# Kernel optimization log

Measured on AMD Instinct MI355X. Metric: run time of the kernel, lower is better.

Reference implementation:

```python
import jax, jax.numpy as jnp
import numpy as np
import math

B, N, D, O, H = 2, 3072, 64, 64, 4

def setup_inputs() -> dict:
    key = jax.random.key(0)
    ks = jax.random.split(key, 8)
    x = jax.random.normal(ks[0], (B, N, D), dtype=jnp.float32)
    edge_index = jax.random.randint(ks[1], (B, N, N), 0, 2, dtype=jnp.int32)
    s = 1.0 / math.sqrt(D)
    Wv = jax.random.uniform(ks[2], (H, D, O), jnp.float32, -s, s)
    bv = jax.random.uniform(ks[3], (H, O), jnp.float32, -s, s)
    Wq = jax.random.uniform(ks[4], (H, D, O), jnp.float32, -s, s)
    bq = jax.random.uniform(ks[5], (H, O), jnp.float32, -s, s)
    Wk = jax.random.uniform(ks[6], (H, D, O), jnp.float32, -s, s)
    bk = jax.random.uniform(ks[7], (H, O), jnp.float32, -s, s)
    return {"x": x, "edge_index": edge_index, "Wv": Wv, "bv": bv,
            "Wq": Wq, "bq": bq, "Wk": Wk, "bk": bk}

def reference(x, edge_index, Wv, bv, Wq, bq, Wk, bk):
    # x: [B,N,D]; edge_index: dense {0,1} adjacency [B,N,N]
    dk = jnp.asarray(math.sqrt(x.shape[-1]), x.dtype)
    v = jnp.einsum('bnd,hdo->bhno', x, Wv) + bv[None, :, None, :]
    q = jnp.einsum('bnd,hdo->bhno', x, Wq) + bq[None, :, None, :]
    k = jnp.einsum('bnd,hdo->bhno', x, Wk) + bk[None, :, None, :]
    scores = jnp.einsum('bhno,bhmo->bhnm', q, k) / dk        # [B,H,N,N]
    scores = jax.nn.leaky_relu(scores, 0.2)
    mask = (-1e10) * (1.0 - edge_index.astype(scores.dtype))  # [B,N,N]
    scores = scores + mask[:, None, :, :]
    prop = jax.nn.softmax(scores, axis=-1)
    # dropout on v omitted (inference mode: identity)
    feats = jnp.einsum('bhnm,bhmo->bhno', prop, v)            # [B,H,N,O]
    out = jnp.mean(feats, axis=1)                             # [B,N,O]
    return jax.nn.leaky_relu(out, 0.2)
```

## Files before the change

### kernel.cpp

```cpp
#include <hip/hip_runtime.h>
#include <hip/hip_bf16.h>
#include <cstdint>

#define Bc 2
#define Nc 3072
#define Hc 4
#define NW32 96
#define TILEB 8192
#define KSC 8
#define TPS (NW32/KSC)

typedef __bf16    bf16x8 __attribute__((ext_vector_type(8)));
typedef _Float16  f16x8  __attribute__((ext_vector_type(8)));
typedef float     f32x16 __attribute__((ext_vector_type(16)));

#define QSCALE 0.18033688f

static __device__ __forceinline__ f32x16 mfma32bf(bf16x8 a, bf16x8 b, f32x16 c) {
    return __builtin_amdgcn_mfma_f32_32x32x16_bf16(a, b, c, 0, 0, 0);
}
static __device__ __forceinline__ f32x16 mfma32h(f16x8 a, f16x8 b, f32x16 c) {
    return __builtin_amdgcn_mfma_f32_32x32x16_f16(a, b, c, 0, 0, 0);
}
static __device__ __forceinline__ uint32_t pkrtz(float lo, float hi) {
    uint32_t w;
    asm("v_cvt_pkrtz_f16_f32 %0, %1, %2" : "=v"(w) : "v"(lo), "v"(hi));
    return w;
}

static __device__ __forceinline__ void softmax_pack(const f32x16& sc, uint32_t mwh,
                                                    uint32_t W8[8], float& lsum,
                                                    uint32_t ones32)
{
    #pragma unroll
    for (int i = 0; i < 8; ++i) {
        const int bp0 = (2*i & 3) + 8*(2*i >> 2);
        float s0 = sc[2*i], s1 = sc[2*i + 1];
        float a0 = fmaxf(s0, 0.2f*s0);
        float a1 = fmaxf(s1, 0.2f*s1);
        float e0, e1;
        asm("v_exp_f32 %0, %1" : "=v"(e0) : "v"(a0));
        asm("v_exp_f32 %0, %1" : "=v"(e1) : "v"(a1));
        uint32_t pk = pkrtz(e0, e1);
        uint32_t m0 = (uint32_t)(((int)(mwh << (31 - bp0))) >> 31);
        uint32_t m1 = (uint32_t)(((int)(mwh << (30 - bp0))) >> 31);
        uint32_t wv = pk & ((m0 & 0x0000ffffu) | (m1 & 0xffff0000u));
        W8[i] = wv;
        asm("v_dot2_f32_f16 %0, %1, %2, %0" : "+v"(lsum) : "v"(wv), "v"(ones32));
    }
}

static __device__ __forceinline__ void assemble_pa(uint32_t W8[8], f16x8& pa0, f16x8& pa1)
{
    uint32_t a0 = W8[0], a2 = W8[2], a1 = W8[1], a3 = W8[3];
    uint32_t b0 = W8[4], b2 = W8[6], b1 = W8[5], b3 = W8[7];
    asm("v_permlane32_swap_b32 %0, %1" : "+v"(a0), "+v"(a2));
    asm("v_permlane32_swap_b32 %0, %1" : "+v"(a1), "+v"(a3));
    asm("v_permlane32_swap_b32 %0, %1" : "+v"(b0), "+v"(b2));
    asm("v_permlane32_swap_b32 %0, %1" : "+v"(b1), "+v"(b3));
    union { uint32_t u[4]; f16x8 v; } u0, u1;
    u0.u[0] = a0; u0.u[1] = a1; u0.u[2] = a2; u0.u[3] = a3;
    u1.u[0] = b0; u1.u[1] = b1; u1.u[2] = b2; u1.u[3] = b3;
    pa0 = u0.v; pa1 = u1.v;
}

static __device__ __forceinline__ void load_subtile(const char* gt, int hi, int l31,
                                                    f16x8 (&K)[4], f16x8 (&V)[4])
{
    #pragma unroll
    for (int kk = 0; kk < 4; ++kk)
        K[kk] = *(const f16x8*)(gt + ((kk*2 + hi) << 9) + (l31 << 4));
    #pragma unroll
    for (int i = 0; i < 4; ++i) {
        const int kkp = i >> 1, ot = i & 1;
        V[i] = *(const f16x8*)(gt + 4096 + ((kkp*2 + hi) << 10) + ((ot*32 + l31) << 4));
    }
}

static __device__ __forceinline__ void compute_subtile(
    const f16x8 (&K)[4], const f16x8 (&V)[4], uint32_t mw, int hi,
    const f16x8 (&qf)[4], const f32x16& fzero, uint32_t ones32,
    f32x16& acc0, f32x16& acc1, float& lsum)
{
    f32x16 sc;
    __builtin_amdgcn_s_setprio(1);
    sc = mfma32h(K[0], qf[0], fzero);
    sc = mfma32h(K[1], qf[1], sc);
    sc = mfma32h(K[2], qf[2], sc);
    sc = mfma32h(K[3], qf[3], sc);
    __builtin_amdgcn_s_setprio(0);

    uint32_t W8[8];
    softmax_pack(sc, mw >> (hi*4), W8, lsum, ones32);
    f16x8 pa0, pa1;
    assemble_pa(W8, pa0, pa1);

    __builtin_amdgcn_s_setprio(1);
    acc0 = mfma32h(pa0, V[0], acc0);
    acc1 = mfma32h(pa0, V[1], acc1);
    acc0 = mfma32h(pa1, V[2], acc0);
    acc1 = mfma32h(pa1, V[3], acc1);
    __builtin_amdgcn_s_setprio(0);
}

__global__ void preppack_kernel(const float* __restrict__ Wq, const float* __restrict__ Wk,
                                const float* __restrict__ Wv,
                                const float* __restrict__ bq, const float* __restrict__ bk,
                                const float* __restrict__ bv,
                                const int* __restrict__ edge,
                                __bf16* __restrict__ Wbh, __bf16* __restrict__ Wbl,
                                float* __restrict__ Bs, uint32_t* __restrict__ pmT)
{
    if (blockIdx.x < 192) {
        int i = blockIdx.x*256 + threadIdx.x;
        int d = i & 63, o = (i >> 6) & 63, h = (i >> 12) & 3, p = i >> 14;
        const float* W = (p == 0) ? Wq : (p == 1) ? Wk : Wv;
        float scale = (p == 0) ? QSCALE : 1.0f;
        float val = W[(h*64 + d)*64 + o] * scale;
        int idx = (((p*Hc + h)*64 + o) << 6) + d;
        __bf16 hi = (__bf16)val;
        Wbh[idx] = hi;
        Wbl[idx] = (__bf16)(val - (float)hi);
        if (i < 3*Hc*64) {
            int pp = i / (Hc*64), rest = i % (Hc*64);
            const float* B = (pp == 0) ? bq : (pp == 1) ? bk : bv;
            Bs[i] = B[rest] * ((pp == 0) ? QSCALE : 1.0f);
        }
    } else {
        int gw = (blockIdx.x - 192)*4 + (threadIdx.x >> 6);
        int lane = threadIdx.x & 63;
        int ng = gw % 48; gw /= 48;
        int w  = gw % NW32; gw /= NW32;
        int b  = gw;
        int n = ng*64 + lane;
        const uint4* ep = (const uint4*)(edge + ((size_t)b*Nc + n)*Nc + w*32);
        uint32_t word = 0;
        #pragma unroll
        for (int i = 0; i < 8; ++i) {
            uint4 e = ep[i];
            word |= (e.x ? 1u : 0u) << (4*i);
            word |= (e.y ? 1u : 0u) << (4*i + 1);
            word |= (e.z ? 1u : 0u) << (4*i + 2);
            word |= (e.w ? 1u : 0u) << (4*i + 3);
        }
        pmT[((size_t)b*NW32 + w)*Nc + n] = word;
    }
}

__global__ __launch_bounds__(256) void qkv_mfma(
    const float* __restrict__ x,
    const __bf16* __restrict__ Wbh, const __bf16* __restrict__ Wbl,
    const float* __restrict__ Bs,
    _Float16* __restrict__ Qf, _Float16* __restrict__ Kf,
    _Float16* __restrict__ KVimg)
{
    const int lane = threadIdx.x & 63, w = threadIdx.x >> 6;
    const int l31 = lane & 31, hi = lane >> 5;
    int t = blockIdx.x;
    int nt = t % 48; t /= 48;
    int b  = t & 1;  t >>= 1;
    int p  = t % 3;
    int h  = t / 3;
    const int r0 = (w >> 1)*32, c0 = (w & 1)*32, n0 = nt*64;

    bf16x8 xh[4], xl[4], wh[4], wl[4];
    #pragma unroll
    for (int kk = 0; kk < 4; ++kk) {
        size_t xoff = (((size_t)(b*Nc + n0 + r0 + l31)) << 6) + kk*16 + hi*8;
        float4 f0 = *(const float4*)(x + xoff);
        float4 f1 = *(const float4*)(x + xoff + 4);
        float xs[8] = {f0.x, f0.y, f0.z, f0.w, f1.x, f1.y, f1.z, f1.w};
        #pragma unroll
        for (int j = 0; j < 8; ++j) {
            __bf16 hh = (__bf16)xs[j];
            xh[kk][j] = hh;
            xl[kk][j] = (__bf16)(xs[j] - (float)hh);
        }
        size_t woff = (((size_t)((p*Hc + h)*64 + c0 + l31)) << 6) + kk*16 + hi*8;
        wh[kk] = *(const bf16x8*)(Wbh + woff);
        wl[kk] = *(const bf16x8*)(Wbl + woff);
    }
    float bias = Bs[(p*Hc + h)*64 + c0 + l31];
    f32x16 acc;
    #pragma unroll
    for (int i = 0; i < 16; ++i) acc[i] = bias;
    #pragma unroll
    for (int kk = 0; kk < 4; ++kk) {
        acc = mfma32bf(xh[kk], wh[kk], acc);
        acc = mfma32bf(xl[kk], wh[kk], acc);
        acc = mfma32bf(xh[kk], wl[kk], acc);
    }
    const int bh = b*Hc + h;
    if (p < 2) {
        _Float16* dst = (p == 0) ? Qf : Kf;
        #pragma unroll
        for (int r = 0; r < 16; ++r) {
            int row = (r & 3) + 8*(r >> 2) + 4*hi;
            size_t idx = (((size_t)bh*Nc + n0 + r0 + row) << 6) + c0 + l31;
            dst[idx] = (_Float16)acc[r];
        }
    } else {
        const int t_img = (n0 + r0) >> 5;
        char* img = (char*)KVimg + (size_t)(bh*96 + t_img)*TILEB;
        #pragma unroll
        for (int grp = 0; grp < 2; ++grp) {
            uint32_t wH[4];
            #pragma unroll
            for (int j = 0; j < 4; ++j)
                wH[j] = pkrtz(acc[grp*8 + 2*j], acc[grp*8 + 2*j + 1]);
            asm("v_permlane32_swap_b32 %0, %1" : "+v"(wH[0]), "+v"(wH[2]));
            asm("v_permlane32_swap_b32 %0, %1" : "+v"(wH[1]), "+v"(wH[3]));
            const int kb = grp*2 + hi;
            const int o  = c0 + l31;
            uint4 gh = {wH[0], wH[1], wH[2], wH[3]};
            *(uint4*)(img + 4096 + ((kb*64 + o) << 4)) = gh;
        }
    }
}

__global__ void imgk_kernel(const _Float16* __restrict__ Kf, _Float16* __restrict__ KVimg)
{
    const int t = blockIdx.x % 96, bh = blockIdx.x / 96;
    char* img = (char*)KVimg + (size_t)(bh*96 + t)*TILEB;
    int dc = threadIdx.x & 7, key = threadIdx.x >> 3;
    size_t src = (((size_t)bh*Nc + t*32 + key) << 6) + dc*8;
    *(uint4*)(img + (dc*32 + key)*16) = *(const uint4*)(Kf + src);
}

__global__ __launch_bounds__(256, 3) void attn_mfma(
    const _Float16* __restrict__ Qf,
    const _Float16* __restrict__ KVimg, const uint32_t* __restrict__ pmT,
    float* __restrict__ PA, float* __restrict__ PL)
{
    const int lane = threadIdx.x & 63, w = threadIdx.x >> 6;
    const int l31 = lane & 31, hi = lane >> 5;
    int gb = blockIdx.x;
    const int bh = gb & 7; gb >>= 3;
    const int qt = gb % 24;
    const int ks = gb / 24;
    const int b = bh >> 2;
    const int qrow0 = qt*128 + w*32;
    const int t0 = ks*TPS;

    const uint32_t* pmp = pmT + ((size_t)b*NW32 + t0)*Nc + qrow0 + l31;
    const char* gt = (const char*)KVimg + (size_t)(bh*96 + t0)*TILEB;

    f16x8 qf[4];
    #pragma unroll
    for (int kk = 0; kk < 4; ++kk) {
        size_t qoff = (((size_t)bh*Nc + qrow0 + l31) << 6) + kk*16 + hi*8;
        qf[kk] = *(const f16x8*)(Qf + qoff);
    }
    f32x16 fzero;
    #pragma unroll
    for (int i = 0; i < 16; ++i) fzero[i] = 0.f;
    const uint32_t ones32 = 0x3C003C00u;

    f32x16 acc0 = fzero, acc1 = fzero;
    float lsum = 0.f;

    f16x8 KA[4], VA[4], KB[4], VB[4];
    uint32_t mwA, mwB;
    load_subtile(gt, hi, l31, KA, VA);
    mwA = pmp[0];

    #pragma unroll 1
    for (int j = 0; j < TPS/2; ++j) {
        load_subtile(gt + (size_t)(2*j + 1)*TILEB, hi, l31, KB, VB);
        mwB = pmp[(size_t)(2*j + 1)*Nc];
        compute_subtile(KA, VA, mwA, hi, qf, fzero, ones32, acc0, acc1, lsum);
        const int tn = (2*j + 2 < TPS) ? (2*j + 2) : 0;
        load_subtile(gt + (size_t)tn*TILEB, hi, l31, KA, VA);
        mwA = pmp[(size_t)tn*Nc];
        compute_subtile(KB, VB, mwB, hi, qf, fzero, ones32, acc0, acc1, lsum);
    }

    lsum += __shfl_xor(lsum, 32);
    float* po = PA + (((size_t)(bh*KSC + ks)*Nc + qrow0) << 6);
    #pragma unroll
    for (int r = 0; r < 16; ++r) {
        int row = (r & 3) + 8*(r >> 2) + 4*hi;
        po[((size_t)row << 6) + l31]      = acc0[r];
        po[((size_t)row << 6) + 32 + l31] = acc1[r];
    }
    if (lane < 32)
        PL[(size_t)(bh*KSC + ks)*Nc + qrow0 + l31] = lsum;
}

__global__ void merge_kernel(const float* __restrict__ PA, const float* __restrict__ PL,
                             float* __restrict__ out)
{
    int gid = blockIdx.x*256 + threadIdx.x;
    int o  = gid & 63;
    int bn = gid >> 6;
    int n  = bn % Nc;
    int b  = bn / Nc;
    float ft = 0.f;
    for (int h = 0; h < Hc; ++h) {
        int bh = b*Hc + h;
        float A = 0.f, L = 0.f;
        for (int ks = 0; ks < KSC; ++ks) {
            A += PA[(((size_t)(bh*KSC + ks)*Nc + n) << 6) + o];
            L += PL[(size_t)(bh*KSC + ks)*Nc + n];
        }
        ft += A / L;
    }
    ft *= 0.25f;
    out[((size_t)bn << 6) + o] = fmaxf(ft, 0.f) + 0.2f*fminf(ft, 0.f);
}

extern "C" void kernel_launch(void* const* d_in, const int* in_sizes, int n_in,
                              void* d_out, int out_size, void* d_ws, size_t ws_size,
                              hipStream_t stream)
{
    const float* x    = (const float*)d_in[0];
    const int*   edge = (const int*)d_in[1];
    const float* Wv   = (const float*)d_in[2];
    const float* bv   = (const float*)d_in[3];
    const float* Wq   = (const float*)d_in[4];
    const float* bq   = (const float*)d_in[5];
    const float* Wk   = (const float*)d_in[6];
    const float* bk   = (const float*)d_in[7];
    float* out = (float*)d_out;

    const size_t PROJ = (size_t)Bc*Hc*Nc*64;
    char* p = (char*)d_ws;
    __bf16* Wbh = (__bf16*)p;     p += 49152*2;
    __bf16* Wbl = (__bf16*)p;     p += 49152*2;
    float*  Bs  = (float*)p;      p += 4096;
    _Float16* Qf = (_Float16*)p;  p += PROJ*2;
    _Float16* Kf = (_Float16*)p;  p += PROJ*2;
    _Float16* KVimg = (_Float16*)p; p += (size_t)Bc*Hc*96*TILEB;
    uint32_t* pmT = (uint32_t*)p; p += (size_t)Bc*NW32*Nc*4;
    float* PA = (float*)p;        p += (size_t)Bc*Hc*KSC*Nc*64*4;
    float* PL = (float*)p;

    hipLaunchKernelGGL(preppack_kernel, dim3(192 + Bc*NW32*48/4), dim3(256), 0, stream,
                       Wq, Wk, Wv, bq, bk, bv, edge, Wbh, Wbl, Bs, pmT);
    hipLaunchKernelGGL(qkv_mfma,    dim3(1152), dim3(256), 0, stream,
                       x, Wbh, Wbl, Bs, Qf, Kf, KVimg);
    hipLaunchKernelGGL(imgk_kernel, dim3(Bc*Hc*96), dim3(256), 0, stream, Kf, KVimg);
    hipLaunchKernelGGL(attn_mfma,   dim3(8*KSC*24), dim3(256), 0, stream,
                       Qf, KVimg, pmT, PA, PL);
    hipLaunchKernelGGL(merge_kernel, dim3((Bc*Nc*64)/256), dim3(256), 0, stream,
                       PA, PL, out);
}
```

Before: 78.86 us.

## Compute softmax row sums with MFMA and halve key split count

The per-lane v_dot2 row-sum accumulation is replaced by two extra MFMAs that multiply the packed probabilities by a ones vector, so the row sums come out in MFMA layout and the final cross-lane shuffle goes away. Mask bit extraction switches to sbfe builtins. The key-split count drops from 8 to 4, so each block handles twice as many tiles and the merge kernel reads less partial data, but fewer blocks are launched. The extra MFMAs add matrix-core work and an extra 16-register accumulator in exchange for fewer VALU ops.

```diff
diff --git a/kernel.cpp b/kernel.cpp
--- a/kernel.cpp
+++ b/kernel.cpp
@@ -7,7 +7,7 @@
 #define Hc 4
 #define NW32 96
 #define TILEB 8192
-#define KSC 8
+#define KSC 4
 #define TPS (NW32/KSC)
 
 typedef __bf16    bf16x8 __attribute__((ext_vector_type(8)));
@@ -29,8 +29,7 @@
 }
 
 static __device__ __forceinline__ void softmax_pack(const f32x16& sc, uint32_t mwh,
-                                                    uint32_t W8[8], float& lsum,
-                                                    uint32_t ones32)
+                                                    uint32_t W8[8])
 {
     #pragma unroll
     for (int i = 0; i < 8; ++i) {
@@ -42,11 +41,10 @@
         asm("v_exp_f32 %0, %1" : "=v"(e0) : "v"(a0));
         asm("v_exp_f32 %0, %1" : "=v"(e1) : "v"(a1));
         uint32_t pk = pkrtz(e0, e1);
-        uint32_t m0 = (uint32_t)(((int)(mwh << (31 - bp0))) >> 31);
-        uint32_t m1 = (uint32_t)(((int)(mwh << (30 - bp0))) >> 31);
-        uint32_t wv = pk & ((m0 & 0x0000ffffu) | (m1 & 0xffff0000u));
-        W8[i] = wv;
-        asm("v_dot2_f32_f16 %0, %1, %2, %0" : "+v"(lsum) : "v"(wv), "v"(ones32));
+        uint32_t m0 = (uint32_t)__builtin_amdgcn_sbfe((int)mwh, bp0, 1);
+        uint32_t m1 = (uint32_t)__builtin_amdgcn_sbfe((int)mwh, bp0 + 1, 1);
+        uint32_t sel = (m0 & 0x0000ffffu) | (m1 & 0xffff0000u);
+        W8[i] = pk & sel;
     }
 }
 
@@ -79,8 +77,8 @@
 
 static __device__ __forceinline__ void compute_subtile(
     const f16x8 (&K)[4], const f16x8 (&V)[4], uint32_t mw, int hi,
-    const f16x8 (&qf)[4], const f32x16& fzero, uint32_t ones32,
-    f32x16& acc0, f32x16& acc1, float& lsum)
+    const f16x8 (&qf)[4], const f32x16& fzero, const f16x8& ones,
+    f32x16& acc0, f32x16& acc1, f32x16& acc2)
 {
     f32x16 sc;
     __builtin_amdgcn_s_setprio(1);
@@ -91,11 +89,13 @@
     __builtin_amdgcn_s_setprio(0);
 
     uint32_t W8[8];
-    softmax_pack(sc, mw >> (hi*4), W8, lsum, ones32);
+    softmax_pack(sc, mw >> (hi*4), W8);
     f16x8 pa0, pa1;
     assemble_pa(W8, pa0, pa1);
 
     __builtin_amdgcn_s_setprio(1);
+    acc2 = mfma32h(pa0, ones, acc2);
+    acc2 = mfma32h(pa1, ones, acc2);
     acc0 = mfma32h(pa0, V[0], acc0);
     acc1 = mfma32h(pa0, V[1], acc1);
     acc0 = mfma32h(pa1, V[2], acc0);
@@ -254,10 +254,11 @@
     f32x16 fzero;
     #pragma unroll
     for (int i = 0; i < 16; ++i) fzero[i] = 0.f;
-    const uint32_t ones32 = 0x3C003C00u;
-
-    f32x16 acc0 = fzero, acc1 = fzero;
-    float lsum = 0.f;
+    f16x8 ones;
+    #pragma unroll
+    for (int j = 0; j < 8; ++j) ones[j] = (_Float16)1.0f;
+
+    f32x16 acc0 = fzero, acc1 = fzero, acc2 = fzero;
 
     f16x8 KA[4], VA[4], KB[4], VB[4];
     uint32_t mwA, mwB;
@@ -268,14 +269,13 @@
     for (int j = 0; j < TPS/2; ++j) {
         load_subtile(gt + (size_t)(2*j + 1)*TILEB, hi, l31, KB, VB);
         mwB = pmp[(size_t)(2*j + 1)*Nc];
-        compute_subtile(KA, VA, mwA, hi, qf, fzero, ones32, acc0, acc1, lsum);
+        compute_subtile(KA, VA, mwA, hi, qf, fzero, ones, acc0, acc1, acc2);
         const int tn = (2*j + 2 < TPS) ? (2*j + 2) : 0;
         load_subtile(gt + (size_t)tn*TILEB, hi, l31, KA, VA);
         mwA = pmp[(size_t)tn*Nc];
-        compute_subtile(KB, VB, mwB, hi, qf, fzero, ones32, acc0, acc1, lsum);
-    }
-
-    lsum += __shfl_xor(lsum, 32);
+        compute_subtile(KB, VB, mwB, hi, qf, fzero, ones, acc0, acc1, acc2);
+    }
+
     float* po = PA + (((size_t)(bh*KSC + ks)*Nc + qrow0) << 6);
     #pragma unroll
     for (int r = 0; r < 16; ++r) {
@@ -283,8 +283,12 @@
         po[((size_t)row << 6) + l31]      = acc0[r];
         po[((size_t)row << 6) + 32 + l31] = acc1[r];
     }
-    if (lane < 32)
-        PL[(size_t)(bh*KSC + ks)*Nc + qrow0 + l31] = lsum;
+    if (l31 == 0) {
+        float* pl = PL + (size_t)(bh*KSC + ks)*Nc + qrow0;
+        #pragma unroll
+        for (int r = 0; r < 16; ++r)
+            pl[(r & 3) + 8*(r >> 2) + 4*hi] = acc2[r];
+    }
 }
 
 __global__ void merge_kernel(const float* __restrict__ PA, const float* __restrict__ PL,
```

Result: faster. 74.56 us (-5.4%).
